# Kernel optimization log

Hardware: AMD Instinct MI355X
Metric: run time of the kernel (lower is better)

The kernel has to match this reference:

```python
import jax, jax.numpy as jnp
import numpy as np

BS, QLEN, DIM, NH = 4, 2048, 1024, 16
DH = DIM // NH
NEG = float(np.finfo(np.float32).min)


def setup_inputs() -> dict:
    key = jax.random.key(0)
    ks = jax.random.split(key, 10)
    s = 1.0 / np.sqrt(DIM)
    return {
        "hidden_states": jax.random.normal(ks[0], (BS, QLEN, DIM), jnp.float32),
        "attention_mask": jnp.ones((BS, QLEN), jnp.int32),
        "Wq": jax.random.normal(ks[1], (DIM, DIM), jnp.float32) * s,
        "bq": jnp.zeros((DIM,), jnp.float32),
        "Wk": jax.random.normal(ks[2], (DIM, DIM), jnp.float32) * s,
        "bk": jnp.zeros((DIM,), jnp.float32),
        "Wv": jax.random.normal(ks[3], (DIM, DIM), jnp.float32) * s,
        "bv": jnp.zeros((DIM,), jnp.float32),
        "Wo": jax.random.normal(ks[4], (DIM, DIM), jnp.float32) * s,
        "bo": jnp.zeros((DIM,), jnp.float32),
    }


def _heads(x, bs):
    # [bs, len, dim] -> [bs, n_heads, len, dim_per_head]
    return x.reshape(bs, -1, NH, DH).transpose(0, 2, 1, 3)


def reference(hidden_states, attention_mask, Wq, bq, Wk, bk, Wv, bv, Wo, bo):
    bs, qlen, dim = hidden_states.shape
    q = _heads(hidden_states @ Wq.T + bq, bs) / jnp.sqrt(jnp.asarray(DH, hidden_states.dtype))
    k = _heads(hidden_states @ Wk.T + bk, bs)
    v = _heads(hidden_states @ Wv.T + bv, bs)
    scores = jnp.einsum("bhqd,bhkd->bhqk", q, k)  # [bs, nh, qlen, klen]
    mask = (attention_mask == 0)[:, None, None, :]  # [bs,1,1,klen]
    scores = jnp.where(mask, NEG, scores)
    weights = jax.nn.softmax(scores.astype(jnp.float32), axis=-1).astype(scores.dtype)
    context = jnp.einsum("bhqk,bhkd->bhqd", weights, v)
    context = context.transpose(0, 2, 1, 3).reshape(bs, qlen, dim)
    return context @ Wo.T + bo
```

## Files before the change

kernel.cpp:

```cpp
#include <hip/hip_runtime.h>
#include <hip/hip_bf16.h>

#define BS 4
#define QLEN 2048
#define DIM 1024
#define NH 16
#define DH 64

typedef __attribute__((ext_vector_type(8))) short bf16x8;
typedef __attribute__((ext_vector_type(4))) float f32x4;
typedef __attribute__((ext_vector_type(16))) float f32x16;
typedef __attribute__((ext_vector_type(2))) unsigned int u32x2;
typedef __attribute__((ext_vector_type(4))) unsigned int u32x4;
typedef unsigned short u16;
typedef unsigned int u32;
typedef unsigned long long u64;

#define LOG2E 1.44269504088896f

__device__ __forceinline__ u32 cvtpk_bf16(float lo, float hi) {
    u32 r;
    asm("v_cvt_pk_bf16_f32 %0, %1, %2" : "=v"(r) : "v"(lo), "v"(hi));
    return r;
}
__device__ __forceinline__ u16 f2bf_hw(float f) { return (u16)cvtpk_bf16(f, f); }

__device__ __forceinline__ void async_lds16(const void* gp, void* lp) {
    __builtin_amdgcn_global_load_lds(
        (const __attribute__((address_space(1))) u32*)(u64)gp,
        (__attribute__((address_space(3))) u32*)(u32)(u64)lp,
        16, 0, 0);
}

__global__ void cvt_fused(const float* __restrict__ H,
                          const float* __restrict__ W0, const float* __restrict__ W1,
                          const float* __restrict__ W2, const float* __restrict__ W3,
                          u16* __restrict__ Hb,
                          u16* __restrict__ D0, u16* __restrict__ D1,
                          u16* __restrict__ D2, u16* __restrict__ D3) {
    const int h4 = (BS * QLEN * DIM) / 4;
    int i = blockIdx.x * blockDim.x + threadIdx.x;
    const float* s;
    u16* d;
    int off;
    if (i < h4) { s = H; d = Hb; off = i; }
    else {
        int j = i - h4;
        int ws = j >> 18;
        off = j & 262143;
        s = ws == 0 ? W0 : ws == 1 ? W1 : ws == 2 ? W2 : W3;
        d = ws == 0 ? D0 : ws == 1 ? D1 : ws == 2 ? D2 : D3;
    }
    float4 v = ((const float4*)s)[off];
    uint2 o;
    o.x = cvtpk_bf16(v.x, v.y);
    o.y = cvtpk_bf16(v.z, v.w);
    ((uint2*)d)[off] = o;
}

__global__ void mask_prep(const int* __restrict__ mask, float* __restrict__ maskF,
                          int* __restrict__ flags) {
    const int tile = blockIdx.x;
    const int lane = threadIdx.x;
    const int idx = tile * 64 + lane;
    const int v = mask[idx];
    maskF[idx] = v ? 1.0f : 0.0f;
    u64 bal = __ballot(v == 0);
    if (lane == 0) flags[tile] = (bal != 0ull) ? 1 : 0;
}

__global__ __launch_bounds__(256) void gemm_qkv(
    const u16* __restrict__ Hb,
    const u16* __restrict__ Wq, const u16* __restrict__ Wk, const u16* __restrict__ Wv,
    const float* __restrict__ bq, const float* __restrict__ bk, const float* __restrict__ bvv,
    u16* __restrict__ Qb, u16* __restrict__ Kb, u16* __restrict__ Vt)
{
    __shared__ __align__(16) u16 As[128 * 32];
    __shared__ __align__(16) u16 Bs[128 * 32];
    const int z = blockIdx.z;
    const u16* W = z == 0 ? Wq : z == 1 ? Wk : Wv;
    const float* bias = z == 0 ? bq : z == 1 ? bk : bvv;
    const int t = threadIdx.x;
    const int w = t >> 6, lane = t & 63;
    const int lr = lane & 15, lg = lane >> 4;
    const int m0 = blockIdx.y * 128, n0 = blockIdx.x * 128;
    const int wm = (w >> 1) * 64, wn = (w & 1) * 64;
    const int srow = w * 16 + (lane >> 2);
    const int sk = (lane & 3) * 8;

    f32x4 acc[4][4] = {};

    for (int kt = 0; kt < DIM; kt += 32) {
        __syncthreads();
        async_lds16(Hb + (u64)(m0 + srow) * DIM + kt + sk,      &As[(w * 16) * 32]);
        async_lds16(Hb + (u64)(m0 + 64 + srow) * DIM + kt + sk, &As[(64 + w * 16) * 32]);
        async_lds16(W + (u64)(n0 + srow) * DIM + kt + sk,       &Bs[(w * 16) * 32]);
        async_lds16(W + (u64)(n0 + 64 + srow) * DIM + kt + sk,  &Bs[(64 + w * 16) * 32]);
        __syncthreads();
        bf16x8 a[4], b[4];
#pragma unroll
        for (int i = 0; i < 4; ++i) a[i] = *(const bf16x8*)&As[(wm + i * 16 + lr) * 32 + lg * 8];
#pragma unroll
        for (int i = 0; i < 4; ++i) b[i] = *(const bf16x8*)&Bs[(wn + i * 16 + lr) * 32 + lg * 8];
#pragma unroll
        for (int mi = 0; mi < 4; ++mi)
#pragma unroll
            for (int ni = 0; ni < 4; ++ni)
                acc[mi][ni] = __builtin_amdgcn_mfma_f32_16x16x32_bf16(a[mi], b[ni], acc[mi][ni], 0, 0, 0);
    }

#pragma unroll
    for (int mi = 0; mi < 4; ++mi)
#pragma unroll
        for (int ni = 0; ni < 4; ++ni) {
            const int col = n0 + wn + ni * 16 + lr;
            const float bb = bias[col];
#pragma unroll
            for (int r = 0; r < 4; ++r) {
                const int row = m0 + wm + mi * 16 + lg * 4 + r;
                const float v = acc[mi][ni][r] + bb;
                const int bh = (row >> 11) * NH + (col >> 6);
                const int q = row & (QLEN - 1);
                const int d = col & (DH - 1);
                if (z == 0)      Qb[((u64)bh * QLEN + q) * DH + d] = f2bf_hw(v * (0.125f * LOG2E));
                else if (z == 1) Kb[((u64)bh * QLEN + q) * DH + d] = f2bf_hw(v);
                else             Vt[((u64)bh * DH + d) * QLEN + q] = f2bf_hw(v);
            }
        }
}

__global__ __launch_bounds__(256) void gemm_o(
    const u16* __restrict__ A, const u16* __restrict__ W,
    const float* __restrict__ bias, float* __restrict__ ofp)
{
    __shared__ __align__(16) u16 As[128 * 32];
    __shared__ __align__(16) u16 Bs[128 * 32];
    const int t = threadIdx.x;
    const int w = t >> 6, lane = t & 63;
    const int lr = lane & 15, lg = lane >> 4;
    const int m0 = blockIdx.y * 128, n0 = blockIdx.x * 128;
    const int wm = (w >> 1) * 64, wn = (w & 1) * 64;
    const int srow = w * 16 + (lane >> 2);
    const int sk = (lane & 3) * 8;

    f32x4 acc[4][4] = {};

    for (int kt = 0; kt < DIM; kt += 32) {
        __syncthreads();
        async_lds16(A + (u64)(m0 + srow) * DIM + kt + sk,      &As[(w * 16) * 32]);
        async_lds16(A + (u64)(m0 + 64 + srow) * DIM + kt + sk, &As[(64 + w * 16) * 32]);
        async_lds16(W + (u64)(n0 + srow) * DIM + kt + sk,      &Bs[(w * 16) * 32]);
        async_lds16(W + (u64)(n0 + 64 + srow) * DIM + kt + sk, &Bs[(64 + w * 16) * 32]);
        __syncthreads();
        bf16x8 a[4], b[4];
#pragma unroll
        for (int i = 0; i < 4; ++i) a[i] = *(const bf16x8*)&As[(wm + i * 16 + lr) * 32 + lg * 8];
#pragma unroll
        for (int i = 0; i < 4; ++i) b[i] = *(const bf16x8*)&Bs[(wn + i * 16 + lr) * 32 + lg * 8];
#pragma unroll
        for (int mi = 0; mi < 4; ++mi)
#pragma unroll
            for (int ni = 0; ni < 4; ++ni)
                acc[mi][ni] = __builtin_amdgcn_mfma_f32_16x16x32_bf16(a[mi], b[ni], acc[mi][ni], 0, 0, 0);
    }

#pragma unroll
    for (int mi = 0; mi < 4; ++mi)
#pragma unroll
        for (int ni = 0; ni < 4; ++ni) {
            const int col = n0 + wn + ni * 16 + lr;
            const float bb = bias[col];
#pragma unroll
            for (int r = 0; r < 4; ++r) {
                const int row = m0 + wm + mi * 16 + lg * 4 + r;
                ofp[(u64)row * DIM + col] = acc[mi][ni][r] + bb;
            }
        }
}

__global__ __launch_bounds__(256, 2) void attn_kernel(
    const u16* __restrict__ Qb, const u16* __restrict__ Kb, const u16* __restrict__ Vt,
    const float* __restrict__ maskF, const int* __restrict__ mflags, u16* __restrict__ ctx)
{
    __shared__ __align__(16) u16 Ks[4][64 * 64];
    __shared__ __align__(16) u16 Vs[4][64 * 64];

    const int t = threadIdx.x;
    const int w = t >> 6, lane = t & 63;
    const int l5 = lane & 31, hi = lane >> 5, l7 = lane & 7;

    const int id = blockIdx.x + 16 * blockIdx.y;
    const int v = (id & 7) * 128 + (id >> 3);
    const int qt = v & 15, bh = v >> 4;
    const int b = bh >> 4, hh = bh & 15;
    const int q0 = qt * 128;

    const u16* Kbh = Kb + (u64)bh * QLEN * DH;
    const u16* Vth = Vt + (u64)bh * DH * QLEN;
    const float* mFb = maskF + b * QLEN;
    const int* flb = mflags + b * (QLEN / 64);

    const u64 fmask = __ballot(flb[lane & 31] != 0);

    const u16* qp = Qb + ((u64)bh * QLEN + q0 + w * 32 + l5) * DH + hi * 8;
    bf16x8 bq[4];
#pragma unroll
    for (int dc = 0; dc < 4; ++dc) bq[dc] = *(const bf16x8*)(qp + dc * 16);

    f32x16 o[2] = {};
    float mrun = -3.0e38f, lsum = 0.f;

    auto STAGE = [&](int B, int KT) {
#pragma unroll
        for (int c = 0; c < 2; ++c) {
            const int row = w * 16 + c * 8 + (lane >> 3);
            const int ch = l7 ^ (row & 7);
            async_lds16(Kbh + (u64)(KT * 64 + row) * DH + ch * 8, &Ks[B][(w * 16 + c * 8) * 64]);
            async_lds16(Vth + (u64)row * QLEN + KT * 64 + ch * 8, &Vs[B][(w * 16 + c * 8) * 64]);
        }
    };

    auto QK = [&](f32x16& s0, f32x16& s1, int B) {
        const char* Kbase = (const char*)&Ks[B][0];
        s0 = f32x16{};
        s1 = f32x16{};
        __builtin_amdgcn_s_setprio(1);
#pragma unroll
        for (int dc = 0; dc < 4; ++dc) {
            const u32 off = (u32)(l5 * 128) + (u32)(((2 * dc + hi) ^ l7) << 4);
            bf16x8 ak0 = *(const bf16x8*)(Kbase + off);
            bf16x8 ak1 = *(const bf16x8*)(Kbase + off + 4096);
            s0 = __builtin_amdgcn_mfma_f32_32x32x16_bf16(ak0, bq[dc], s0, 0, 0, 0);
            s1 = __builtin_amdgcn_mfma_f32_32x32x16_bf16(ak1, bq[dc], s1, 0, 0, 0);
        }
        __builtin_amdgcn_s_setprio(0);
    };

    auto SMPV = [&](f32x16& s0, f32x16& s1, int B, int kt64) {
        const char* Vbase = (const char*)&Vs[B][0];

        bf16x8 av0[4], av1[4];
#pragma unroll
        for (int kc = 0; kc < 4; ++kc) {
            const u32 voff = (u32)(l5 * 128) + (u32)(((2 * kc + hi) ^ l7) << 4);
            av0[kc] = *(const bf16x8*)(Vbase + voff);
            av1[kc] = *(const bf16x8*)(Vbase + voff + 4096);
        }

        float mx[16];
#pragma unroll
        for (int i = 0; i < 16; ++i) mx[i] = fmaxf(s0[i], s1[i]);
#pragma unroll
        for (int st = 8; st > 0; st >>= 1)
#pragma unroll
            for (int i = 0; i < 16; ++i) if (i < st) mx[i] = fmaxf(mx[i], mx[i + st]);
        const float tma = fmaxf(mx[0], __shfl_xor(mx[0], 32));

        if (!__all(tma <= mrun + 11.5415603f)) {
            const float nm = fmaxf(mrun, tma);
            const float corr = exp2f(mrun - nm);
            mrun = nm;
            lsum *= corr;
#pragma unroll
            for (int i = 0; i < 16; ++i) { o[0][i] *= corr; o[1][i] *= corr; }
        }

#pragma unroll
        for (int i = 0; i < 16; ++i) {
            s0[i] = exp2f(s0[i] - mrun);
            s1[i] = exp2f(s1[i] - mrun);
        }

        if ((fmask >> kt64) & 1ull) {
#pragma unroll
            for (int kb = 0; kb < 2; ++kb) {
                f32x16& sk = kb == 0 ? s0 : s1;
#pragma unroll
                for (int m = 0; m < 4; ++m) {
                    float4 mm = *(const float4*)&mFb[kt64 * 64 + kb * 32 + m * 8 + hi * 4];
                    sk[4 * m + 0] *= mm.x;
                    sk[4 * m + 1] *= mm.y;
                    sk[4 * m + 2] *= mm.z;
                    sk[4 * m + 3] *= mm.w;
                }
            }
        }

        {
            float ps[16];
#pragma unroll
            for (int i = 0; i < 16; ++i) ps[i] = s0[i] + s1[i];
#pragma unroll
            for (int st = 8; st > 0; st >>= 1)
#pragma unroll
                for (int i = 0; i < 16; ++i) if (i < st) ps[i] += ps[i + st];
            lsum += ps[0];
        }

        __builtin_amdgcn_s_setprio(1);
#pragma unroll
        for (int kc = 0; kc < 4; ++kc) {
            const f32x16& sk = (kc >> 1) == 0 ? s0 : s1;
            const int base = 8 * (kc & 1);
            const u32 P00 = cvtpk_bf16(sk[base + 0], sk[base + 1]);
            const u32 P01 = cvtpk_bf16(sk[base + 2], sk[base + 3]);
            const u32 P10 = cvtpk_bf16(sk[base + 4], sk[base + 5]);
            const u32 P11 = cvtpk_bf16(sk[base + 6], sk[base + 7]);
            u32x2 w02 = __builtin_amdgcn_permlane32_swap(P00, P10, false, false);
            u32x2 w13 = __builtin_amdgcn_permlane32_swap(P01, P11, false, false);
            u32x4 words;
            words.x = w02[0]; words.y = w13[0]; words.z = w02[1]; words.w = w13[1];
            const bf16x8 bp = __builtin_bit_cast(bf16x8, words);

            o[0] = __builtin_amdgcn_mfma_f32_32x32x16_bf16(av0[kc], bp, o[0], 0, 0, 0);
            o[1] = __builtin_amdgcn_mfma_f32_32x32x16_bf16(av1[kc], bp, o[1], 0, 0, 0);
        }
        __builtin_amdgcn_s_setprio(0);
    };

    f32x16 sX0, sX1, sY0, sY1;

    STAGE(0, 0);
    STAGE(1, 1);
    STAGE(2, 2);
    asm volatile("s_waitcnt vmcnt(8)" ::: "memory");
    __builtin_amdgcn_s_barrier();
    __builtin_amdgcn_sched_barrier(0);
    QK(sX0, sX1, 0);

    for (int tt = 0; tt < 30; tt += 2) {
        asm volatile("s_waitcnt vmcnt(4)" ::: "memory");
        __builtin_amdgcn_s_barrier();
        __builtin_amdgcn_sched_barrier(0);
        if (tt + 3 < 32) STAGE((tt + 3) & 3, tt + 3);
        QK(sY0, sY1, (tt + 1) & 3);
        SMPV(sX0, sX1, tt & 3, tt);
        asm volatile("s_waitcnt vmcnt(4)" ::: "memory");
        __builtin_amdgcn_s_barrier();
        __builtin_amdgcn_sched_barrier(0);
        if (tt + 4 < 32) STAGE((tt + 4) & 3, tt + 4);
        QK(sX0, sX1, (tt + 2) & 3);
        SMPV(sY0, sY1, (tt + 1) & 3, tt + 1);
    }
    asm volatile("s_waitcnt vmcnt(0)" ::: "memory");
    __builtin_amdgcn_s_barrier();
    __builtin_amdgcn_sched_barrier(0);
    QK(sY0, sY1, 31 & 3);
    SMPV(sX0, sX1, 30 & 3, 30);
    SMPV(sY0, sY1, 31 & 3, 31);

    const float lall = lsum + __shfl_xor(lsum, 32);
    const float inv = 1.0f / fmaxf(lall, 1e-37f);

    u16* cp = ctx + (((u64)b * QLEN + (q0 + w * 32 + l5)) * NH + hh) * DH;
#pragma unroll
    for (int db = 0; db < 2; ++db)
#pragma unroll
        for (int m = 0; m < 4; ++m) {
            const int d0 = db * 32 + m * 8 + hi * 4;
            const u32 wA = cvtpk_bf16(o[db][4 * m + 0] * inv, o[db][4 * m + 1] * inv);
            const u32 wB = cvtpk_bf16(o[db][4 * m + 2] * inv, o[db][4 * m + 3] * inv);
            *(u32*)(cp + d0) = wA;
            *(u32*)(cp + d0 + 2) = wB;
        }
}

extern "C" void kernel_launch(void* const* d_in, const int* in_sizes, int n_in,
                              void* d_out, int out_size, void* d_ws, size_t ws_size,
                              hipStream_t stream) {
    const float* H    = (const float*)d_in[0];
    const int*   mask = (const int*)d_in[1];
    const float* Wq   = (const float*)d_in[2];
    const float* bq   = (const float*)d_in[3];
    const float* Wk   = (const float*)d_in[4];
    const float* bk   = (const float*)d_in[5];
    const float* Wv   = (const float*)d_in[6];
    const float* bv   = (const float*)d_in[7];
    const float* Wo   = (const float*)d_in[8];
    const float* bo   = (const float*)d_in[9];
    float* out = (float*)d_out;

    const u64 NTOK = (u64)BS * QLEN;
    const u64 HN = NTOK * DIM;
    const u64 WN = (u64)DIM * DIM;

    u16* Hb  = (u16*)d_ws;
    u16* Wqb = Hb + HN;
    u16* Wkb = Wqb + WN;
    u16* Wvb = Wkb + WN;
    u16* Wob = Wvb + WN;
    u16* Qb  = Wob + WN;
    u16* Kb  = Qb + HN;
    u16* Vtg = Kb + HN;
    u16* Ctx = Vtg + HN;
    float* maskF = (float*)(Ctx + HN);
    int* mflags = (int*)(maskF + BS * QLEN);

    cvt_fused<<<12288, 256, 0, stream>>>(H, Wq, Wk, Wv, Wo, Hb, Wqb, Wkb, Wvb, Wob);
    mask_prep<<<BS * (QLEN / 64), 64, 0, stream>>>(mask, maskF, mflags);

    gemm_qkv<<<dim3(DIM / 128, (int)(NTOK / 128), 3), 256, 0, stream>>>(
        Hb, Wqb, Wkb, Wvb, bq, bk, bv, Qb, Kb, Vtg);

    attn_kernel<<<dim3(QLEN / 128, BS * NH), 256, 0, stream>>>(Qb, Kb, Vtg, maskF, mflags, Ctx);

    gemm_o<<<dim3(DIM / 128, (int)(NTOK / 128)), 256, 0, stream>>>(Ctx, Wob, bo, out);
}
```

Measured before the change: 252.6 us.

## Store K/V in MFMA fragment order and load directly to registers in attention

The QKV GEMM epilogue now writes K and V in a pre-swizzled fragment-major layout, so each lane's MFMA operand is a contiguous 16-byte chunk. The attention kernel drops the LDS staging, barriers and async copies, and loads K/V fragments straight from global memory into registers with a simple double-buffered K prefetch. This removes LDS traffic and synchronisation. In exchange, the four waves in a block each fetch the same K/V from global/L2 rather than sharing them, V loads are not prefetched, and the scattered epilogue stores may cost more. The launch-bounds occupancy hint is also removed.

Result: faster. 240.2 us (-4.9%).

```diff
diff --git a/kernel.cpp b/kernel.cpp
--- a/kernel.cpp
+++ b/kernel.cpp
@@ -73,7 +73,7 @@
     const u16* __restrict__ Hb,
     const u16* __restrict__ Wq, const u16* __restrict__ Wk, const u16* __restrict__ Wv,
     const float* __restrict__ bq, const float* __restrict__ bk, const float* __restrict__ bvv,
-    u16* __restrict__ Qb, u16* __restrict__ Kb, u16* __restrict__ Vt)
+    u16* __restrict__ Qb, u16* __restrict__ KF, u16* __restrict__ VF)
 {
     __shared__ __align__(16) u16 As[128 * 32];
     __shared__ __align__(16) u16 Bs[128 * 32];
@@ -122,9 +122,20 @@
                 const int bh = (row >> 11) * NH + (col >> 6);
                 const int q = row & (QLEN - 1);
                 const int d = col & (DH - 1);
-                if (z == 0)      Qb[((u64)bh * QLEN + q) * DH + d] = f2bf_hw(v * (0.125f * LOG2E));
-                else if (z == 1) Kb[((u64)bh * QLEN + q) * DH + d] = f2bf_hw(v);
-                else             Vt[((u64)bh * DH + d) * QLEN + q] = f2bf_hw(v);
+                if (z == 0) {
+                    Qb[((u64)bh * QLEN + q) * DH + d] = f2bf_hw(v * (0.125f * LOG2E));
+                } else if (z == 1) {
+                    const int ktile = q >> 6, kb2 = (q >> 5) & 1, kl5 = q & 31;
+                    const int c = d >> 3, dcc = c >> 1, chi = c & 1, j = d & 7;
+                    KF[(u64)bh * QLEN * DH +
+                       ((((u64)ktile * 2 + kb2) * 4 + dcc) * 64 + chi * 32 + kl5) * 8 + j] = f2bf_hw(v);
+                } else {
+                    const int ktile = q >> 6, kin = q & 63;
+                    const int c = kin >> 3, kcc = c >> 1, chi = c & 1, j = kin & 7;
+                    const int db = d >> 5, vl5 = d & 31;
+                    VF[(u64)bh * QLEN * DH +
+                       ((((u64)ktile * 2 + db) * 4 + kcc) * 64 + chi * 32 + vl5) * 8 + j] = f2bf_hw(v);
+                }
             }
         }
 }
@@ -178,16 +189,15 @@
         }
 }
 
-__global__ __launch_bounds__(256, 2) void attn_kernel(
-    const u16* __restrict__ Qb, const u16* __restrict__ Kb, const u16* __restrict__ Vt,
+struct KTile { bf16x8 f[2][4]; };
+
+__global__ __launch_bounds__(256) void attn_kernel(
+    const u16* __restrict__ Qb, const u16* __restrict__ KF, const u16* __restrict__ VF,
     const float* __restrict__ maskF, const int* __restrict__ mflags, u16* __restrict__ ctx)
 {
-    __shared__ __align__(16) u16 Ks[4][64 * 64];
-    __shared__ __align__(16) u16 Vs[4][64 * 64];
-
     const int t = threadIdx.x;
     const int w = t >> 6, lane = t & 63;
-    const int l5 = lane & 31, hi = lane >> 5, l7 = lane & 7;
+    const int l5 = lane & 31, hi = lane >> 5;
 
     const int id = blockIdx.x + 16 * blockIdx.y;
     const int v = (id & 7) * 128 + (id >> 3);
@@ -195,11 +205,10 @@
     const int b = bh >> 4, hh = bh & 15;
     const int q0 = qt * 128;
 
-    const u16* Kbh = Kb + (u64)bh * QLEN * DH;
-    const u16* Vth = Vt + (u64)bh * DH * QLEN;
+    const u16* kfl = KF + (u64)bh * QLEN * DH + (u64)lane * 8;
+    const u16* vfl = VF + (u64)bh * QLEN * DH + (u64)lane * 8;
     const float* mFb = maskF + b * QLEN;
     const int* flb = mflags + b * (QLEN / 64);
-
     const u64 fmask = __ballot(flb[lane & 31] != 0);
 
     const u16* qp = Qb + ((u64)bh * QLEN + q0 + w * 32 + l5) * DH + hi * 8;
@@ -210,42 +219,32 @@
     f32x16 o[2] = {};
     float mrun = -3.0e38f, lsum = 0.f;
 
-    auto STAGE = [&](int B, int KT) {
-#pragma unroll
-        for (int c = 0; c < 2; ++c) {
-            const int row = w * 16 + c * 8 + (lane >> 3);
-            const int ch = l7 ^ (row & 7);
-            async_lds16(Kbh + (u64)(KT * 64 + row) * DH + ch * 8, &Ks[B][(w * 16 + c * 8) * 64]);
-            async_lds16(Vth + (u64)row * QLEN + KT * 64 + ch * 8, &Vs[B][(w * 16 + c * 8) * 64]);
-        }
+    auto loadK = [&](KTile& kk, int KT) {
+        const u16* base = kfl + (u64)KT * 4096;
+#pragma unroll
+        for (int kb = 0; kb < 2; ++kb)
+#pragma unroll
+            for (int dc = 0; dc < 4; ++dc)
+                kk.f[kb][dc] = *(const bf16x8*)(base + (kb * 4 + dc) * 512);
     };
 
-    auto QK = [&](f32x16& s0, f32x16& s1, int B) {
-        const char* Kbase = (const char*)&Ks[B][0];
-        s0 = f32x16{};
-        s1 = f32x16{};
+    auto tile = [&](const KTile& kk, int kt64) {
+        const u16* vb = vfl + (u64)kt64 * 4096;
+        bf16x8 av0[4], av1[4];
+#pragma unroll
+        for (int kc = 0; kc < 4; ++kc) {
+            av0[kc] = *(const bf16x8*)(vb + kc * 512);
+            av1[kc] = *(const bf16x8*)(vb + (4 + kc) * 512);
+        }
+
+        f32x16 s0 = {}, s1 = {};
         __builtin_amdgcn_s_setprio(1);
 #pragma unroll
         for (int dc = 0; dc < 4; ++dc) {
-            const u32 off = (u32)(l5 * 128) + (u32)(((2 * dc + hi) ^ l7) << 4);
-            bf16x8 ak0 = *(const bf16x8*)(Kbase + off);
-            bf16x8 ak1 = *(const bf16x8*)(Kbase + off + 4096);
-            s0 = __builtin_amdgcn_mfma_f32_32x32x16_bf16(ak0, bq[dc], s0, 0, 0, 0);
-            s1 = __builtin_amdgcn_mfma_f32_32x32x16_bf16(ak1, bq[dc], s1, 0, 0, 0);
+            s0 = __builtin_amdgcn_mfma_f32_32x32x16_bf16(kk.f[0][dc], bq[dc], s0, 0, 0, 0);
+            s1 = __builtin_amdgcn_mfma_f32_32x32x16_bf16(kk.f[1][dc], bq[dc], s1, 0, 0, 0);
         }
         __builtin_amdgcn_s_setprio(0);
-    };
-
-    auto SMPV = [&](f32x16& s0, f32x16& s1, int B, int kt64) {
-        const char* Vbase = (const char*)&Vs[B][0];
-
-        bf16x8 av0[4], av1[4];
-#pragma unroll
-        for (int kc = 0; kc < 4; ++kc) {
-            const u32 voff = (u32)(l5 * 128) + (u32)(((2 * kc + hi) ^ l7) << 4);
-            av0[kc] = *(const bf16x8*)(Vbase + voff);
-            av1[kc] = *(const bf16x8*)(Vbase + voff + 4096);
-        }
 
         float mx[16];
 #pragma unroll
@@ -318,36 +317,14 @@
         __builtin_amdgcn_s_setprio(0);
     };
 
-    f32x16 sX0, sX1, sY0, sY1;
-
-    STAGE(0, 0);
-    STAGE(1, 1);
-    STAGE(2, 2);
-    asm volatile("s_waitcnt vmcnt(8)" ::: "memory");
-    __builtin_amdgcn_s_barrier();
-    __builtin_amdgcn_sched_barrier(0);
-    QK(sX0, sX1, 0);
-
-    for (int tt = 0; tt < 30; tt += 2) {
-        asm volatile("s_waitcnt vmcnt(4)" ::: "memory");
-        __builtin_amdgcn_s_barrier();
-        __builtin_amdgcn_sched_barrier(0);
-        if (tt + 3 < 32) STAGE((tt + 3) & 3, tt + 3);
-        QK(sY0, sY1, (tt + 1) & 3);
-        SMPV(sX0, sX1, tt & 3, tt);
-        asm volatile("s_waitcnt vmcnt(4)" ::: "memory");
-        __builtin_amdgcn_s_barrier();
-        __builtin_amdgcn_sched_barrier(0);
-        if (tt + 4 < 32) STAGE((tt + 4) & 3, tt + 4);
-        QK(sX0, sX1, (tt + 2) & 3);
-        SMPV(sY0, sY1, (tt + 1) & 3, tt + 1);
+    KTile kA, kB;
+    loadK(kA, 0);
+    for (int tt = 0; tt < 32; tt += 2) {
+        loadK(kB, tt + 1);
+        tile(kA, tt);
+        if (tt + 2 < 32) loadK(kA, tt + 2);
+        tile(kB, tt + 1);
     }
-    asm volatile("s_waitcnt vmcnt(0)" ::: "memory");
-    __builtin_amdgcn_s_barrier();
-    __builtin_amdgcn_sched_barrier(0);
-    QK(sY0, sY1, 31 & 3);
-    SMPV(sX0, sX1, 30 & 3, 30);
-    SMPV(sY0, sY1, 31 & 3, 31);
 
     const float lall = lsum + __shfl_xor(lsum, 32);
     const float inv = 1.0f / fmaxf(lall, 1e-37f);
@@ -390,9 +367,9 @@
     u16* Wvb = Wkb + WN;
     u16* Wob = Wvb + WN;
     u16* Qb  = Wob + WN;
-    u16* Kb  = Qb + HN;
-    u16* Vtg = Kb + HN;
-    u16* Ctx = Vtg + HN;
+    u16* KFb = Qb + HN;
+    u16* VFb = KFb + HN;
+    u16* Ctx = VFb + HN;
     float* maskF = (float*)(Ctx + HN);
     int* mflags = (int*)(maskF + BS * QLEN);
 
@@ -400,9 +377,9 @@
     mask_prep<<<BS * (QLEN / 64), 64, 0, stream>>>(mask, maskF, mflags);
 
     gemm_qkv<<<dim3(DIM / 128, (int)(NTOK / 128), 3), 256, 0, stream>>>(
-        Hb, Wqb, Wkb, Wvb, bq, bk, bv, Qb, Kb, Vtg);
-
-    attn_kernel<<<dim3(QLEN / 128, BS * NH), 256, 0, stream>>>(Qb, Kb, Vtg, maskF, mflags, Ctx);
+        Hb, Wqb, Wkb, Wvb, bq, bk, bv, Qb, KFb, VFb);
+
+    attn_kernel<<<dim3(QLEN / 128, BS * NH), 256, 0, stream>>>(Qb, KFb, VFb, maskF, mflags, Ctx);
 
     gemm_o<<<dim3(DIM / 128, (int)(NTOK / 128)), 256, 0, stream>>>(Ctx, Wob, bo, out);
 }
```
